# Performance work log

Measured on AMD Instinct MI355X. Metric: run time of the kernel, lower is better.

Reference implementation:

```python
import jax, jax.numpy as jnp
import numpy as np

N_NODES = 100000
N_EDGES = 1600000


def gcn_conv(x, src, dst, w, W, b, n_nodes):
    # PyG GCNConv: linear -> add self-loops (weight 1) -> symmetric norm -> scatter-add -> bias
    h = x @ W  # [N, out]
    loop = jnp.arange(n_nodes, dtype=src.dtype)
    s = jnp.concatenate([src, loop])
    d = jnp.concatenate([dst, loop])
    ew = jnp.concatenate([w, jnp.ones((n_nodes,), dtype=w.dtype)])
    deg = jax.ops.segment_sum(ew, d, num_segments=n_nodes)  # weighted in-degree (incl. self-loop)
    dis = jnp.where(deg > 0, jax.lax.rsqrt(deg), 0.0)
    norm = dis[s] * ew * dis[d]  # [E+N]
    msgs = norm[:, None] * h[s]  # gather source features, scale per edge
    out = jax.ops.segment_sum(msgs, d, num_segments=n_nodes)  # scatter-add at destinations
    return out + b


def setup_inputs() -> dict:
    key = jax.random.key(0)
    ks = jax.random.split(key, 6)
    x = jax.random.normal(ks[0], (N_NODES, 128), dtype=jnp.float32)
    edge_index = jax.random.randint(ks[1], (2, N_EDGES), 0, N_NODES, dtype=jnp.int32)
    edge_weight = jax.random.uniform(ks[2], (N_EDGES,), dtype=jnp.float32)
    W1 = jax.random.normal(ks[3], (128, 64), dtype=jnp.float32) * (1.0 / np.sqrt(128))
    b1 = jnp.zeros((64,), dtype=jnp.float32)
    W2 = jax.random.normal(ks[4], (64, 16), dtype=jnp.float32) * (1.0 / np.sqrt(64))
    b2 = jnp.zeros((16,), dtype=jnp.float32)
    return {"x": x, "edge_index": edge_index, "edge_weight": edge_weight,
            "W1": W1, "b1": b1, "W2": W2, "b2": b2}


def reference(x, edge_index, edge_weight, W1, b1, W2, b2):
    src, dst = edge_index[0], edge_index[1]
    x_emb = gcn_conv(x, src, dst, edge_weight, W1, b1, N_NODES)
    h = jax.nn.relu(x_emb)  # dropout is identity in eval mode
    out = gcn_conv(h, src, dst, edge_weight, W2, b2, N_NODES)
    return (out, x_emb)
```

## Files before the change

kernel.cpp:

```cpp
#include <hip/hip_runtime.h>

#define NN 100000
#define NE 1600000
#define BSH 7
#define BSZ 128
#define NBKT 782
#define CAP 2560
#define NPB 256
#define EPB 6250

typedef unsigned short u16;
typedef unsigned int   u32;
typedef unsigned long long u64;
typedef __attribute__((ext_vector_type(8))) __bf16 bf16x8;
typedef __attribute__((ext_vector_type(4))) float  f32x4;

__device__ __forceinline__ float bf2f(u16 u) {
    union { u32 i; float f; } v; v.i = ((u32)u) << 16; return v.f;
}
__device__ __forceinline__ u16 f2bf(float f) {
    union { float f; u32 i; } v; v.f = f;
    u32 u = v.i;
    u += 0x7FFFu + ((u >> 16) & 1);
    return (u16)(u >> 16);
}
__device__ __forceinline__ float bfLO(u32 p) { return __uint_as_float(p << 16); }
__device__ __forceinline__ float bfHI(u32 p) { return __uint_as_float(p & 0xffff0000u); }
__device__ __forceinline__ u64 nt_load_u64(const uint2* p) {
    return __builtin_nontemporal_load((const u64*)p);
}

__global__ __launch_bounds__(256) void k_wpack(const float* __restrict__ W1,
                                               const float* __restrict__ W2,
                                               bf16x8* __restrict__ wp1,
                                               bf16x8* __restrict__ wp2,
                                               int* __restrict__ cursor,
                                               int* __restrict__ gctr) {
    int t = threadIdx.x;
    #pragma unroll
    for (int s = 0; s < 4; ++s) {
        int idx = s * 256 + t;
        int q = idx >> 6, l = idx & 63;
        int kb = q >> 2, ct = q & 3;
        int k0 = kb * 32 + ((l >> 4) * 8);
        int c  = ct * 16 + (l & 15);
        bf16x8 v;
        #pragma unroll
        for (int i = 0; i < 8; ++i) v[i] = (__bf16)W1[(k0 + i) * 64 + c];
        wp1[idx] = v;
    }
    if (t < 128) {
        int q = t >> 6, l = t & 63;
        int k0 = q * 32 + ((l >> 4) * 8);
        int c  = l & 15;
        bf16x8 v;
        #pragma unroll
        for (int i = 0; i < 8; ++i) v[i] = (__bf16)W2[(k0 + i) * 16 + c];
        wp2[t] = v;
    }
    for (int i = t; i < NBKT; i += 256) cursor[i] = i * CAP;
    if (t == 0) *gctr = 0;
}

__global__ __launch_bounds__(1024) void k_part(const int* __restrict__ src,
                                               const int* __restrict__ dst,
                                               const float* __restrict__ w,
                                               int* __restrict__ cursor,
                                               uint2* __restrict__ rec) {
    __shared__ int cnt[NBKT];
    __shared__ int base[NBKT];
    int tid = threadIdx.x;
    for (int i = tid; i < NBKT; i += 1024) cnt[i] = 0;
    __syncthreads();
    int e0 = blockIdx.x * EPB;
    for (int j = tid; j < EPB; j += 1024)
        atomicAdd(&cnt[dst[e0 + j] >> BSH], 1);
    __syncthreads();
    for (int i = tid; i < NBKT; i += 1024) {
        int c = cnt[i];
        base[i] = c ? atomicAdd(&cursor[i], c) : 0;
    }
    __syncthreads();
    for (int i = tid; i < NBKT; i += 1024) cnt[i] = 0;
    __syncthreads();
    for (int j = tid; j < EPB; j += 1024) {
        int e  = e0 + j;
        int d  = dst[e];
        int bk = d >> BSH;
        int slot = base[bk] + atomicAdd(&cnt[bk], 1);
        rec[slot] = make_uint2(__float_as_uint(w[e]),
                               ((u32)src[e] << BSH) | (u32)(d & (BSZ - 1)));
    }
}

__global__ __launch_bounds__(512) void k_build(const int* __restrict__ cursor,
                                               const uint2* __restrict__ rec,
                                               uint2* __restrict__ rec2,
                                               float* __restrict__ dis,
                                               int2* __restrict__ rowinfo,
                                               int* __restrict__ gctr) {
    __shared__ float dw[BSZ];
    __shared__ int   cnt[BSZ];
    __shared__ int   base[BSZ];
    __shared__ int   scn[BSZ];
    __shared__ float disl[BSZ];
    __shared__ int   sh_gbase;
    int b = blockIdx.x, tid = threadIdx.x;
    int s = b * CAP;
    int total = cursor[b] - s;
    if (tid < BSZ) { dw[tid] = 1.0f; cnt[tid] = 0; }
    if (tid == 0) sh_gbase = atomicAdd(gctr, total);
    __syncthreads();
    for (int j = tid; j < total; j += 512) {
        uint2 r = rec[s + j];
        int dl = r.y & (BSZ - 1);
        atomicAdd(&cnt[dl], 1);
        atomicAdd(&dw[dl], __uint_as_float(r.x));
    }
    __syncthreads();
    if (tid < BSZ) scn[tid] = cnt[tid];
    __syncthreads();
    #pragma unroll
    for (int off = 1; off < BSZ; off <<= 1) {
        int add = (tid < BSZ && tid >= off) ? scn[tid - off] : 0;
        __syncthreads();
        if (tid < BSZ) scn[tid] += add;
        __syncthreads();
    }
    int gbase = sh_gbase;
    if (tid < BSZ) {
        int node = b * BSZ + tid;
        base[tid] = (tid == 0) ? 0 : scn[tid - 1];
        float d = rsqrtf(dw[tid]);
        disl[tid] = d;
        if (node < NN) {
            dis[node] = d;
            rowinfo[node] = make_int2(gbase + base[tid], gbase + base[tid] + cnt[tid]);
        }
        cnt[tid] = 0;
    }
    __syncthreads();
    for (int j = tid; j < total; j += 512) {
        uint2 r = rec[s + j];
        int dl = r.y & (BSZ - 1);
        int pos = gbase + base[dl] + atomicAdd(&cnt[dl], 1);
        rec2[pos] = make_uint2(__float_as_uint(__uint_as_float(r.x) * disl[dl]),
                               r.y >> BSH);
    }
}

__global__ __launch_bounds__(256) void k_gemm1(const float* __restrict__ x,
                                               const bf16x8* __restrict__ wp1,
                                               const float* __restrict__ dis,
                                               u16* __restrict__ h1b) {
    int tid  = threadIdx.x;
    int lane = tid & 63;
    int wave = tid >> 6;
    int r0   = blockIdx.x * 64 + wave * 16;

    bf16x8 bfrag[16];
    #pragma unroll
    for (int q = 0; q < 16; ++q) bfrag[q] = wp1[q * 64 + lane];

    int  arow = r0 + (lane & 15);
    bool aok  = arow < NN;
    const float* xrow = x + (size_t)arow * 128 + ((lane >> 4) * 8);

    f32x4 acc0 = {0,0,0,0}, acc1 = {0,0,0,0}, acc2 = {0,0,0,0}, acc3 = {0,0,0,0};
    #pragma unroll
    for (int kb = 0; kb < 4; ++kb) {
        f32x4 xlo = {0,0,0,0}, xhi = {0,0,0,0};
        if (aok) {
            xlo = *(const f32x4*)(xrow + kb * 32);
            xhi = *(const f32x4*)(xrow + kb * 32 + 4);
        }
        bf16x8 a;
        a[0] = (__bf16)xlo[0]; a[1] = (__bf16)xlo[1]; a[2] = (__bf16)xlo[2]; a[3] = (__bf16)xlo[3];
        a[4] = (__bf16)xhi[0]; a[5] = (__bf16)xhi[1]; a[6] = (__bf16)xhi[2]; a[7] = (__bf16)xhi[3];
        acc0 = __builtin_amdgcn_mfma_f32_16x16x32_bf16(a, bfrag[kb * 4 + 0], acc0, 0, 0, 0);
        acc1 = __builtin_amdgcn_mfma_f32_16x16x32_bf16(a, bfrag[kb * 4 + 1], acc1, 0, 0, 0);
        acc2 = __builtin_amdgcn_mfma_f32_16x16x32_bf16(a, bfrag[kb * 4 + 2], acc2, 0, 0, 0);
        acc3 = __builtin_amdgcn_mfma_f32_16x16x32_bf16(a, bfrag[kb * 4 + 3], acc3, 0, 0, 0);
    }

    int rbase = r0 + (lane >> 4) * 4;
    int cbase = lane & 15;
    #pragma unroll
    for (int reg = 0; reg < 4; ++reg) {
        int row = rbase + reg;
        if (row < NN) {
            float d = dis[row];
            u16* hp = h1b + (size_t)row * 64 + cbase;
            hp[0]  = f2bf(acc0[reg] * d);
            hp[16] = f2bf(acc1[reg] * d);
            hp[32] = f2bf(acc2[reg] * d);
            hp[48] = f2bf(acc3[reg] * d);
        }
    }
}

#define ACC8(hv, nrm) { \
    a0 = fmaf(nrm, bfLO(hv.x), a0); a1 = fmaf(nrm, bfHI(hv.x), a1); \
    a2 = fmaf(nrm, bfLO(hv.y), a2); a3 = fmaf(nrm, bfHI(hv.y), a3); \
    a4 = fmaf(nrm, bfLO(hv.z), a4); a5 = fmaf(nrm, bfHI(hv.z), a5); \
    a6 = fmaf(nrm, bfLO(hv.w), a6); a7 = fmaf(nrm, bfHI(hv.w), a7); }

__global__ __launch_bounds__(512) void k_agg1(const int2* __restrict__ rowinfo,
                                              const uint2* __restrict__ rec2,
                                              const u16* __restrict__ h1b,
                                              const float* __restrict__ dis,
                                              const float* __restrict__ b1,
                                              float* __restrict__ xemb) {
    int n    = blockIdx.x * 8 + (threadIdx.x >> 6);
    int lane = threadIdx.x & 63;
    int el   = lane >> 3;
    int f8   = (lane & 7) * 8;
    int2 ri  = rowinfo[n];
    int beg = ri.x, end = ri.y;

    float a0=0,a1=0,a2=0,a3=0,a4=0,a5=0,a6=0,a7=0;

    u64 p0 = 0, p1 = 0;
    if (beg + el < end)     p0 = nt_load_u64(&rec2[beg + el]);
    if (beg + 8 + el < end) p1 = nt_load_u64(&rec2[beg + 8 + el]);

    for (int j = beg; j < end; j += 16) {
        u64 q0 = 0, q1 = 0;
        if (j + 16 + el < end) q0 = nt_load_u64(&rec2[j + 16 + el]);
        if (j + 24 + el < end) q1 = nt_load_u64(&rec2[j + 24 + el]);
        if (j + el < end) {
            u32 srcn = (u32)(p0 >> 32);
            float nrm = __uint_as_float((u32)p0);
            uint4 hv = *(const uint4*)(h1b + (size_t)srcn * 64 + f8);
            ACC8(hv, nrm);
        }
        if (j + 8 + el < end) {
            u32 srcn = (u32)(p1 >> 32);
            float nrm = __uint_as_float((u32)p1);
            uint4 hv = *(const uint4*)(h1b + (size_t)srcn * 64 + f8);
            ACC8(hv, nrm);
        }
        p0 = q0; p1 = q1;
    }

    #pragma unroll
    for (int m = 8; m <= 32; m <<= 1) {
        a0 += __shfl_xor(a0, m, 64); a1 += __shfl_xor(a1, m, 64);
        a2 += __shfl_xor(a2, m, 64); a3 += __shfl_xor(a3, m, 64);
        a4 += __shfl_xor(a4, m, 64); a5 += __shfl_xor(a5, m, 64);
        a6 += __shfl_xor(a6, m, 64); a7 += __shfl_xor(a7, m, 64);
    }
    if (el == 0) {
        float di = dis[n];
        uint4 hv = *(const uint4*)(h1b + (size_t)n * 64 + f8);
        f32x4 lo, hi;
        lo[0] = fmaf(di, bfLO(hv.x), b1[f8 + 0]) + a0;
        lo[1] = fmaf(di, bfHI(hv.x), b1[f8 + 1]) + a1;
        lo[2] = fmaf(di, bfLO(hv.y), b1[f8 + 2]) + a2;
        lo[3] = fmaf(di, bfHI(hv.y), b1[f8 + 3]) + a3;
        hi[0] = fmaf(di, bfLO(hv.z), b1[f8 + 4]) + a4;
        hi[1] = fmaf(di, bfHI(hv.z), b1[f8 + 5]) + a5;
        hi[2] = fmaf(di, bfLO(hv.w), b1[f8 + 6]) + a6;
        hi[3] = fmaf(di, bfHI(hv.w), b1[f8 + 7]) + a7;
        f32x4* dst0 = (f32x4*)&xemb[(size_t)n * 64 + f8];
        __builtin_nontemporal_store(lo, dst0);
        __builtin_nontemporal_store(hi, dst0 + 1);
    }
}

__global__ __launch_bounds__(256) void k_gemm2(const float* __restrict__ xemb,
                                               const bf16x8* __restrict__ wp2,
                                               const float* __restrict__ dis,
                                               u16* __restrict__ h3b) {
    int tid  = threadIdx.x;
    int lane = tid & 63;
    int wave = tid >> 6;
    int r0   = blockIdx.x * 64 + wave * 16;

    bf16x8 b0 = wp2[lane], b1 = wp2[64 + lane];

    int  arow = r0 + (lane & 15);
    bool aok  = arow < NN;
    const float* xrow = xemb + (size_t)arow * 64 + ((lane >> 4) * 8);

    f32x4 acc = {0,0,0,0};
    #pragma unroll
    for (int kb = 0; kb < 2; ++kb) {
        f32x4 xlo = {0,0,0,0}, xhi = {0,0,0,0};
        if (aok) {
            xlo = *(const f32x4*)(xrow + kb * 32);
            xhi = *(const f32x4*)(xrow + kb * 32 + 4);
        }
        bf16x8 a;
        #pragma unroll
        for (int i = 0; i < 4; ++i) {
            float lo = xlo[i] > 0.f ? xlo[i] : 0.f;
            float hi = xhi[i] > 0.f ? xhi[i] : 0.f;
            a[i]     = (__bf16)lo;
            a[i + 4] = (__bf16)hi;
        }
        acc = __builtin_amdgcn_mfma_f32_16x16x32_bf16(a, kb == 0 ? b0 : b1, acc, 0, 0, 0);
    }

    int rbase = r0 + (lane >> 4) * 4;
    int cbase = lane & 15;
    #pragma unroll
    for (int reg = 0; reg < 4; ++reg) {
        int row = rbase + reg;
        if (row < NN)
            h3b[(size_t)row * 16 + cbase] = f2bf(acc[reg] * dis[row]);
    }
}

__global__ __launch_bounds__(512) void k_agg2(const int2* __restrict__ rowinfo,
                                              const uint2* __restrict__ rec2,
                                              const u16* __restrict__ h3b,
                                              const float* __restrict__ dis,
                                              const float* __restrict__ b2,
                                              float* __restrict__ out) {
    int n    = blockIdx.x * 8 + (threadIdx.x >> 6);
    int lane = threadIdx.x & 63;
    int el   = lane >> 2;
    int f4   = (lane & 3) * 4;
    int2 ri  = rowinfo[n];
    int beg = ri.x, end = ri.y;

    float a0=0,a1=0,a2=0,a3=0;

    u64 p0 = 0, p1 = 0;
    if (beg + el < end)      p0 = nt_load_u64(&rec2[beg + el]);
    if (beg + 16 + el < end) p1 = nt_load_u64(&rec2[beg + 16 + el]);

    for (int j = beg; j < end; j += 32) {
        u64 q0 = 0, q1 = 0;
        if (j + 32 + el < end) q0 = nt_load_u64(&rec2[j + 32 + el]);
        if (j + 48 + el < end) q1 = nt_load_u64(&rec2[j + 48 + el]);
        if (j + el < end) {
            u32 srcn = (u32)(p0 >> 32);
            float nrm = __uint_as_float((u32)p0);
            uint2 hv = *(const uint2*)(h3b + (size_t)srcn * 16 + f4);
            a0 = fmaf(nrm, bfLO(hv.x), a0); a1 = fmaf(nrm, bfHI(hv.x), a1);
            a2 = fmaf(nrm, bfLO(hv.y), a2); a3 = fmaf(nrm, bfHI(hv.y), a3);
        }
        if (j + 16 + el < end) {
            u32 srcn = (u32)(p1 >> 32);
            float nrm = __uint_as_float((u32)p1);
            uint2 hv = *(const uint2*)(h3b + (size_t)srcn * 16 + f4);
            a0 = fmaf(nrm, bfLO(hv.x), a0); a1 = fmaf(nrm, bfHI(hv.x), a1);
            a2 = fmaf(nrm, bfLO(hv.y), a2); a3 = fmaf(nrm, bfHI(hv.y), a3);
        }
        p0 = q0; p1 = q1;
    }

    #pragma unroll
    for (int m = 4; m <= 32; m <<= 1) {
        a0 += __shfl_xor(a0, m, 64);
        a1 += __shfl_xor(a1, m, 64);
        a2 += __shfl_xor(a2, m, 64);
        a3 += __shfl_xor(a3, m, 64);
    }
    if (lane < 4) {
        float di = dis[n];
        uint2 hv = *(const uint2*)(h3b + (size_t)n * 16 + f4);
        float4 bb = *(const float4*)&b2[f4];
        float4 r;
        r.x = fmaf(di, bfLO(hv.x), bb.x) + a0;
        r.y = fmaf(di, bfHI(hv.x), bb.y) + a1;
        r.z = fmaf(di, bfLO(hv.y), bb.z) + a2;
        r.w = fmaf(di, bfHI(hv.y), bb.w) + a3;
        *(float4*)&out[(size_t)n * 16 + f4] = r;
    }
}

extern "C" void kernel_launch(void* const* d_in, const int* in_sizes, int n_in,
                              void* d_out, int out_size, void* d_ws, size_t ws_size,
                              hipStream_t stream) {
    const float* x  = (const float*)d_in[0];
    const int*   ei = (const int*)d_in[1];
    const float* w  = (const float*)d_in[2];
    const float* W1 = (const float*)d_in[3];
    const float* b1 = (const float*)d_in[4];
    const float* W2 = (const float*)d_in[5];
    const float* b2 = (const float*)d_in[6];
    const int* src = ei;
    const int* dst = ei + NE;

    float* out2 = (float*)d_out;
    float* xemb = (float*)d_out + NN * 16;

    uint2*  rec_pad = (uint2*)d_ws;
    u16*    h1b     = (u16*)d_ws;
    uint2*  rec2    = rec_pad + (size_t)NBKT * CAP;
    u16*    h3b     = (u16*)(rec2 + NE);
    bf16x8* wp1     = (bf16x8*)(h3b + (size_t)NN * 16);
    bf16x8* wp2     = wp1 + 1024;
    float*  dis     = (float*)(wp2 + 128);
    int2*   rowinfo = (int2*)(dis + NN);
    int*    cursor  = (int*)(rowinfo + NN);
    int*    gctr    = cursor + NBKT;

    k_wpack<<<1,     256, 0, stream>>>(W1, W2, wp1, wp2, cursor, gctr);
    k_part <<<NPB,  1024, 0, stream>>>(src, dst, w, cursor, rec_pad);
    k_build<<<NBKT,  512, 0, stream>>>(cursor, rec_pad, rec2, dis, rowinfo, gctr);

    k_gemm1<<<(NN + 63) / 64, 256, 0, stream>>>(x, wp1, dis, h1b);
    k_agg1 <<<NN / 8, 512, 0, stream>>>(rowinfo, rec2, h1b, dis, b1, xemb);

    k_gemm2<<<(NN + 63) / 64, 256, 0, stream>>>(xemb, wp2, dis, h3b);
    k_agg2 <<<NN / 8, 512, 0, stream>>>(rowinfo, rec2, h3b, dis, b2, out2);
}
```

Before: 165.5 us.

## Stage partitioned edges in LDS for coalesced writes and deepen agg1 gather prefetch

The partition kernel now sorts each block's edges by bucket in shared memory using a local prefix scan, then writes them out to global memory in contiguous runs instead of scattering single records with per-edge atomics. The first aggregation kernel software-pipelines one level deeper, issuing feature-row gathers for the next 16 edges and record loads for the 16 after, all before accumulating the current ones. This is meant to improve write coalescing and hide gather latency. The cost is much more LDS in the partition kernel (about 64KB), a 10-step scan with many barriers, and more live registers in the aggregation loop.

```diff
diff --git a/kernel.cpp b/kernel.cpp
--- a/kernel.cpp
+++ b/kernel.cpp
@@ -67,29 +67,52 @@
                                                const float* __restrict__ w,
                                                int* __restrict__ cursor,
                                                uint2* __restrict__ rec) {
-    __shared__ int cnt[NBKT];
-    __shared__ int base[NBKT];
+    __shared__ uint2 sedge[EPB];
+    __shared__ u16   sbkt[EPB];
+    __shared__ int   cnt[NBKT];
+    __shared__ int   lstart[NBKT];
+    __shared__ int   gbase[NBKT];
+    __shared__ int   scanbuf[1024];
     int tid = threadIdx.x;
+    int e0  = blockIdx.x * EPB;
+
     for (int i = tid; i < NBKT; i += 1024) cnt[i] = 0;
     __syncthreads();
-    int e0 = blockIdx.x * EPB;
     for (int j = tid; j < EPB; j += 1024)
         atomicAdd(&cnt[dst[e0 + j] >> BSH], 1);
     __syncthreads();
+    int v = (tid < NBKT) ? cnt[tid] : 0;
+    scanbuf[tid] = v;
+    __syncthreads();
+    #pragma unroll
+    for (int off = 1; off < 1024; off <<= 1) {
+        int add = (tid >= off) ? scanbuf[tid - off] : 0;
+        __syncthreads();
+        scanbuf[tid] += add;
+        __syncthreads();
+    }
+    if (tid < NBKT) lstart[tid] = scanbuf[tid] - v;
+    __syncthreads();
     for (int i = tid; i < NBKT; i += 1024) {
         int c = cnt[i];
-        base[i] = c ? atomicAdd(&cursor[i], c) : 0;
-    }
-    __syncthreads();
-    for (int i = tid; i < NBKT; i += 1024) cnt[i] = 0;
+        gbase[i] = c ? atomicAdd(&cursor[i], c) : 0;
+        cnt[i] = 0;
+    }
     __syncthreads();
     for (int j = tid; j < EPB; j += 1024) {
         int e  = e0 + j;
         int d  = dst[e];
         int bk = d >> BSH;
-        int slot = base[bk] + atomicAdd(&cnt[bk], 1);
-        rec[slot] = make_uint2(__float_as_uint(w[e]),
-                               ((u32)src[e] << BSH) | (u32)(d & (BSZ - 1)));
+        int slot = lstart[bk] + atomicAdd(&cnt[bk], 1);
+        sedge[slot] = make_uint2(__float_as_uint(w[e]),
+                                 ((u32)src[e] << BSH) | (u32)(d & (BSZ - 1)));
+        sbkt[slot]  = (u16)bk;
+    }
+    __syncthreads();
+    for (int j = tid; j < EPB; j += 1024) {
+        int bk   = sbkt[j];
+        int dest = gbase[bk] + (j - lstart[bk]);
+        rec[dest] = sedge[j];
     }
 }
 
@@ -220,27 +243,42 @@
 
     float a0=0,a1=0,a2=0,a3=0,a4=0,a5=0,a6=0,a7=0;
 
-    u64 p0 = 0, p1 = 0;
-    if (beg + el < end)     p0 = nt_load_u64(&rec2[beg + el]);
-    if (beg + 8 + el < end) p1 = nt_load_u64(&rec2[beg + 8 + el]);
+    int j0 = beg + el;
+    u64 r0 = 0, r1 = 0, r2 = 0, r3 = 0;
+    if (j0 < end)      r0 = nt_load_u64(&rec2[j0]);
+    if (j0 + 8 < end)  r1 = nt_load_u64(&rec2[j0 + 8]);
+    if (j0 + 16 < end) r2 = nt_load_u64(&rec2[j0 + 16]);
+    if (j0 + 24 < end) r3 = nt_load_u64(&rec2[j0 + 24]);
+    uint4 g0 = {0,0,0,0}, g1 = {0,0,0,0};
+    float n0 = 0.f, n1 = 0.f;
+    if (j0 < end) {
+        g0 = *(const uint4*)(h1b + (size_t)(u32)(r0 >> 32) * 64 + f8);
+        n0 = __uint_as_float((u32)r0);
+    }
+    if (j0 + 8 < end) {
+        g1 = *(const uint4*)(h1b + (size_t)(u32)(r1 >> 32) * 64 + f8);
+        n1 = __uint_as_float((u32)r1);
+    }
 
     for (int j = beg; j < end; j += 16) {
-        u64 q0 = 0, q1 = 0;
-        if (j + 16 + el < end) q0 = nt_load_u64(&rec2[j + 16 + el]);
-        if (j + 24 + el < end) q1 = nt_load_u64(&rec2[j + 24 + el]);
-        if (j + el < end) {
-            u32 srcn = (u32)(p0 >> 32);
-            float nrm = __uint_as_float((u32)p0);
-            uint4 hv = *(const uint4*)(h1b + (size_t)srcn * 64 + f8);
-            ACC8(hv, nrm);
-        }
-        if (j + 8 + el < end) {
-            u32 srcn = (u32)(p1 >> 32);
-            float nrm = __uint_as_float((u32)p1);
-            uint4 hv = *(const uint4*)(h1b + (size_t)srcn * 64 + f8);
-            ACC8(hv, nrm);
-        }
-        p0 = q0; p1 = q1;
+        uint4 h2 = {0,0,0,0}, h3 = {0,0,0,0};
+        float n2 = 0.f, n3 = 0.f;
+        if (j0 + 16 < end) {
+            h2 = *(const uint4*)(h1b + (size_t)(u32)(r2 >> 32) * 64 + f8);
+            n2 = __uint_as_float((u32)r2);
+        }
+        if (j0 + 24 < end) {
+            h3 = *(const uint4*)(h1b + (size_t)(u32)(r3 >> 32) * 64 + f8);
+            n3 = __uint_as_float((u32)r3);
+        }
+        u64 nr0 = 0, nr1 = 0;
+        if (j0 + 32 < end) nr0 = nt_load_u64(&rec2[j0 + 32]);
+        if (j0 + 40 < end) nr1 = nt_load_u64(&rec2[j0 + 40]);
+        ACC8(g0, n0);
+        ACC8(g1, n1);
+        g0 = h2; n0 = n2; g1 = h3; n1 = n3;
+        r0 = r2; r1 = r3; r2 = nr0; r3 = nr1;
+        j0 += 16;
     }
 
     #pragma unroll
```

New measurement: 160.1 us. 3.3% less time.
